# Performance work log

Measured on AMD Instinct MI355X. Metric: run time of the kernel, lower is better.

Reference implementation:

```python
import jax, jax.numpy as jnp
from jax import lax
import numpy as np

IMG_H = 14; IMG_W = 14
L = 21   # num_labels
M = 5    # num_mixture_filters
KL = 50  # local conv kernel
PL = 25  # local conv padding
HO = IMG_H + 2 * PL - KL + 1  # 15, locally-connected output size
CH = [(64, 3), (64, 64), (128, 64), (128, 128), (256, 128), (256, 256), (256, 256),
      (512, 256), (512, 512), (512, 512), (512, 512), (512, 512), (512, 512)]
DIL = [1, 1, 1, 1, 1, 1, 1, 1, 1, 1, 2, 2, 2]


def setup_inputs() -> dict:
    keys = iter(jax.random.split(jax.random.key(0), 80))
    def rnd(shape, s=0.05):
        return jax.random.normal(next(keys), shape, dtype=jnp.float32) * s
    d = {"x": jax.random.normal(next(keys), (2, 3, IMG_H, IMG_W), dtype=jnp.float32)}
    for i, (o, c) in enumerate(CH):
        d["w%d" % (i + 1)] = rnd((o, c, 3, 3))
        d["b%d" % (i + 1)] = rnd((o,))
    d["wf1"] = rnd((4096, 512, 7, 7), s=0.01); d["bf1"] = rnd((4096,))
    d["wf2"] = rnd((4096, 4096, 1, 1), s=0.01); d["bf2"] = rnd((4096,))
    d["wf3"] = rnd((L, 4096, 1, 1), s=0.01); d["bf3"] = rnd((L,))
    d["wl"] = rnd((HO, HO, L, L, KL, KL), s=0.01)  # per-position local-conv weights
    d["bl"] = rnd((L, HO, HO))
    d["wa"] = rnd((L, L)); d["ba"] = rnd((L,))
    d["wm"] = rnd((L * M, L, 9, 9, L)); d["bm"] = rnd((L * M,))
    d["wb"] = rnd((L * M, L * M)); d["bb"] = rnd((L * M,))
    return d


def _conv2d(x, w, b, pad, dil=1):
    y = lax.conv_general_dilated(x, w, (1, 1), [(pad, pad), (pad, pad)],
                                 rhs_dilation=(dil, dil),
                                 dimension_numbers=("NCHW", "OIHW", "NCHW"))
    return y + b[None, :, None, None]


def _maxpool2(x):
    return lax.reduce_window(x, -jnp.inf, lax.max, (1, 1, 2, 2), (1, 1, 2, 2), "VALID")


def _upsample_bilinear_ac(x, H, W):
    # UpsamplingBilinear2d == bilinear with align_corners=True
    def lerp(t, n_in, n_out, axis):
        src = jnp.arange(n_out, dtype=jnp.float32) * (float(n_in - 1) / max(n_out - 1, 1))
        i0 = jnp.clip(jnp.floor(src).astype(jnp.int32), 0, max(n_in - 2, 0))
        i1 = jnp.minimum(i0 + 1, n_in - 1)
        f = src - i0.astype(jnp.float32)
        shp = [1] * t.ndim; shp[axis] = n_out
        f = f.reshape(shp).astype(t.dtype)
        return jnp.take(t, i0, axis=axis) * (1 - f) + jnp.take(t, i1, axis=axis) * f
    return lerp(lerp(x, x.shape[2], H, 2), x.shape[3], W, 3)


def reference(x, w1, b1, w2, b2, w3, b3, w4, b4, w5, b5, w6, b6, w7, b7, w8, b8,
              w9, b9, w10, b10, w11, b11, w12, b12, w13, b13,
              wf1, bf1, wf2, bf2, wf3, bf3, wl, bl, wa, ba, wm, bm, wb, bb):
    ws = [w1, w2, w3, w4, w5, w6, w7, w8, w9, w10, w11, w12, w13]
    bs = [b1, b2, b3, b4, b5, b6, b7, b8, b9, b10, b11, b12, b13]
    h = x
    for i in range(13):
        h = jax.nn.relu(_conv2d(h, ws[i], bs[i], pad=DIL[i], dil=DIL[i]))
        if i in (1, 3, 6):  # MaxPool2d after VGG blocks 1,2,3
            h = _maxpool2(h)
    h = jax.nn.relu(_conv2d(h, wf1, bf1, pad=12, dil=4))  # 7x7 dilated FC-conv
    h = jax.nn.relu(_conv2d(h, wf2, bf2, pad=0))
    h = _conv2d(h, wf3, bf3, pad=0)                       # -> [B, L, h', w']
    h = jax.nn.sigmoid(_upsample_bilinear_ac(h, IMG_H, IMG_W))
    # Conv2dLocal: locally-connected 50x50 conv, per-position weights
    xp = jnp.pad(h, ((0, 0), (0, 0), (PL, PL), (PL, PL)))
    idx = jnp.arange(HO)[:, None] + jnp.arange(KL)[None, :]  # [HO, KL]
    p = xp[:, :, idx, :][:, :, :, :, idx]  # [B, C, HO, KL, HO, KL]
    h = jnp.einsum("bcisjt,ijocst->boij", p, wl) + bl[None]  # [B, L, HO, HO]
    # Linear over the label (channel) axis
    h = jnp.einsum("bchw,oc->bohw", h, wa) + ba[None, :, None, None]
    # Conv3d mixture head: label axis unsqueezed to depth-1 last spatial dim,
    # kernel (9, 9, L) with padding (4, 4, L//2) -> depth out = 1
    y = lax.conv_general_dilated(h[..., None], wm, (1, 1, 1),
                                 [(4, 4), (4, 4), (L // 2, L // 2)],
                                 dimension_numbers=("NCDHW", "OIDHW", "NCDHW"))
    h = y[..., 0] + bm[None, :, None, None]  # [B, L*M, HO, HO]
    h = jnp.einsum("bchw,oc->bohw", h, wb) + bb[None, :, None, None]
    # BlockMinPooling(kernel=M) over last dim: split into (M, W//M), min over block axis
    B_, C_, H_, W_ = h.shape
    h = h.reshape(B_, C_, H_, M, W_ // M).min(axis=3)  # [B, L*M, HO, HO//M]
    # AvgPool2d(kernel=1, stride=1, divisor_override=1) is the identity
    return jax.nn.softmax(h, axis=1)
```

## Files before the change

kernel.cpp:

```cpp
#include <hip/hip_runtime.h>
#include <math.h>

#define HO 15
#define LBL 21
#define MIX 5
#define LM 105
#define NB 256
#define NT 256
#define GSZ (NB * NT)
#define NWV (GSZ / 64)

struct Params {
    const float* x;
    const float* w[14]; const float* b[14];
    const float *wf1, *bf1, *wf2, *bf2, *wf3, *bf3;
    const float *wl, *bl, *wa, *ba, *wm, *bm, *wb, *bb;
    float *A, *B, *v, *h1, *h3, *out;
    float *wf1d, *wtd[6], *wmd;
    int* bar;
};

__device__ __forceinline__ float max4(float a, float b, float c, float d) {
    return fmaxf(fmaxf(a, b), fmaxf(c, d));
}

__device__ __forceinline__ void gbar(int* bar, int id) {
    __syncthreads();
    if (threadIdx.x == 0) {
        __threadfence();
        int* c = bar + id * 16;
        __hip_atomic_fetch_add(c, 1, __ATOMIC_RELAXED, __HIP_MEMORY_SCOPE_AGENT);
        while (__hip_atomic_load(c, __ATOMIC_RELAXED, __HIP_MEMORY_SCOPE_AGENT) < NB)
            __builtin_amdgcn_s_sleep(16);
        (void)__hip_atomic_load(c, __ATOMIC_ACQUIRE, __HIP_MEMORY_SCOPE_AGENT);
    }
    __syncthreads();
}

__device__ void extract(const float* __restrict__ src, float* __restrict__ dst,
                        int n, int stride, int off, int gtid) {
#pragma unroll 4
    for (int e = gtid; e < n; e += GSZ) dst[e] = src[(size_t)e * stride + off];
}

template <int Cin, int Cout, int Hi, int H, int POOL>
__device__ void wconv(const float* __restrict__ in, const float* __restrict__ w,
                      const float* __restrict__ bias, float* __restrict__ out,
                      int gw, int lane) {
    constexpr int CPL = Cin / 64;
    for (int idx = gw; idx < 2 * Cout * H * H; idx += NWV) {
        int x = idx % H; int t = idx / H;
        int y = t % H; t /= H;
        int o = t % Cout; int b = t / Cout;
        const float* ip = in + (size_t)b * Cin * Hi * Hi;
        float acc = 0.f;
#pragma unroll
        for (int cc = 0; cc < CPL; ++cc) {
            int c = lane + 64 * cc;
            const float* ic = ip + (size_t)c * Hi * Hi;
            const float* wc = w + ((size_t)o * Cin + c) * 9;
#pragma unroll
            for (int ky = 0; ky < 3; ++ky) {
                int yy = y + ky - 1;
                if (yy < 0 || yy >= H) continue;
#pragma unroll
                for (int kx = 0; kx < 3; ++kx) {
                    int xx = x + kx - 1;
                    if (xx < 0 || xx >= H) continue;
                    float val;
                    if (POOL == 1) {
                        val = ic[yy * Hi + xx];
                    } else {
                        const float* q = ic + (2 * yy) * Hi + 2 * xx;
                        val = max4(q[0], q[1], q[Hi], q[Hi + 1]);
                    }
                    acc += val * wc[ky * 3 + kx];
                }
            }
        }
#pragma unroll
        for (int off = 32; off; off >>= 1) acc += __shfl_xor(acc, off);
        if (lane == 0) out[idx] = fmaxf(acc + bias[o], 0.f);
    }
}

template <int Cin, int ACT, int POOLIN>
__device__ void mvdense(const float* __restrict__ in, const float* __restrict__ wd,
                        const float* __restrict__ bias, float* __restrict__ out,
                        int Cout, float* sin, int tid, int gw, int lane) {
    if (POOLIN) {
        for (int c = tid; c < 2 * Cin; c += NT) {
            const float* q = in + (size_t)c * 9;
            sin[c] = max4(q[0], q[1], q[3], q[4]);
        }
    } else {
        for (int c = tid; c < 2 * Cin; c += NT) sin[c] = in[c];
    }
    __syncthreads();
    constexpr int K = Cin / 64;
    for (int o = gw; o < Cout; o += NWV) {
        const float* wp = wd + (size_t)o * Cin + lane;
        float wr[K];
#pragma unroll
        for (int k = 0; k < K; ++k) wr[k] = wp[64 * k];
        float a0 = 0.f, a1 = 0.f;
#pragma unroll
        for (int k = 0; k < K; ++k) {
            a0 += wr[k] * sin[lane + 64 * k];
            a1 += wr[k] * sin[Cin + lane + 64 * k];
        }
#pragma unroll
        for (int off = 32; off; off >>= 1) {
            a0 += __shfl_xor(a0, off);
            a1 += __shfl_xor(a1, off);
        }
        if (lane == 0) {
            float bv = bias[o];
            a0 += bv; a1 += bv;
            if (ACT == 1) { a0 = fmaxf(a0, 0.f); a1 = fmaxf(a1, 0.f); }
            if (ACT == 2) { a0 = 1.f / (1.f + expf(-a0)); a1 = 1.f / (1.f + expf(-a1)); }
            out[o] = a0;
            out[Cout + o] = a1;
        }
    }
}

__device__ void localstage(const float* __restrict__ wl, const float* __restrict__ bl,
                           const float* __restrict__ v, float* __restrict__ h1,
                           int gw, int lane) {
    int e1 = lane + 64, e2 = lane + 128, e3 = lane + 192;
    int off0 = (lane / 14) * 50 + lane % 14;
    int off1 = (e1 / 14) * 50 + e1 % 14;
    int off2 = (e2 / 14) * 50 + e2 % 14;
    int off3 = (lane < 4) ? ((e3 / 14) * 50 + e3 % 14) : off0;
    float m3 = (lane < 4) ? 1.f : 0.f;
    for (int wk = gw; wk < LBL * HO * HO; wk += NWV) {
        int j = wk % HO; int t1 = wk / HO;
        int i = t1 % HO; int o = t1 / HO;
        int s0 = 25 - i, t0 = 25 - j;
        size_t base_ij = ((size_t)(i * HO + j) * LBL + o) * LBL;
        const float* pij = wl + base_ij * 2500 + s0 * 50 + t0;
        float a0 = 0.f, a1 = 0.f;
#pragma unroll 7
        for (int c = 0; c < LBL; ++c) {
            const float* p = pij + (size_t)c * 2500;
            float part = p[off0] + p[off1] + p[off2] + m3 * p[off3];
            a0 += v[c] * part;
            a1 += v[LBL + c] * part;
        }
#pragma unroll
        for (int off = 32; off; off >>= 1) {
            a0 += __shfl_xor(a0, off);
            a1 += __shfl_xor(a1, off);
        }
        if (lane == 0) {
            float bv = bl[(o * HO + i) * HO + j];
            h1[(size_t)(0 * LBL + o) * 225 + i * HO + j] = a0 + bv;
            h1[(size_t)(1 * LBL + o) * 225 + i * HO + j] = a1 + bv;
        }
    }
}

__device__ void ninestage(const float* __restrict__ h1, const float* __restrict__ wa,
                          const float* __restrict__ ba, const float* __restrict__ wmd,
                          const float* __restrict__ bm, float* __restrict__ h3,
                          float* smem, int tid) {
    int blk = blockIdx.x;
    if (blk >= 2 * LM) return;
    float* s1 = smem;
    float* s2 = smem + 4725;
    float* sw = smem + 9450;
    float* swa = smem + 11151;
    int b = blk / LM, o = blk % LM;
    for (int k = tid; k < 4725; k += NT) s1[k] = h1[(size_t)b * 4725 + k];
    for (int k = tid; k < 441; k += NT) swa[k] = wa[k];
    for (int k = tid; k < 1701; k += NT) sw[k] = wmd[(size_t)o * 1701 + k];
    __syncthreads();
    for (int k = tid; k < 4725; k += NT) {
        int c = k / 225, pix = k % 225;
        float acc = ba[c];
#pragma unroll 7
        for (int c2 = 0; c2 < LBL; ++c2)
            acc += swa[c * LBL + c2] * s1[c2 * 225 + pix];
        s2[k] = acc;
    }
    __syncthreads();
    if (tid >= 225) return;
    int i = tid / HO, j = tid % HO;
    float acc = bm[o];
    for (int c = 0; c < LBL; ++c) {
        const float* wp = sw + c * 81;
        const float* hp = s2 + c * 225;
#pragma unroll
        for (int di = 0; di < 9; ++di) {
            int y = i + di - 4;
            if (y < 0 || y >= HO) continue;
#pragma unroll
            for (int dj = 0; dj < 9; ++dj) {
                int x = j + dj - 4;
                if (x < 0 || x >= HO) continue;
                acc += hp[y * HO + x] * wp[di * 9 + dj];
            }
        }
    }
    h3[((size_t)b * LM + o) * 225 + tid] = acc;
}

__device__ void finalstage(const float* __restrict__ h3, const float* __restrict__ wbw,
                           const float* __restrict__ bbv, float* __restrict__ out,
                           float* smem, int tid) {
    int blk = blockIdx.x;
    if (blk >= 2 * HO * 3) return;
    float* sv = smem;
    float* sred = smem + 112;
    int k = blk % 3; int t = blk / 3; int i = t % HO; int b = t / HO;
    int o = tid;
    if (o < LM) {
        float mn = 3.4e38f;
        for (int mm = 0; mm < MIX; ++mm) {
            int j = mm * 3 + k;
            float acc = bbv[o];
            const float* hp = h3 + (size_t)b * LM * 225 + i * HO + j;
            const float* wp = wbw + o * LM;
#pragma unroll 5
            for (int c = 0; c < LM; ++c) acc += wp[c] * hp[(size_t)c * 225];
            mn = fminf(mn, acc);
        }
        sv[o] = mn;
    }
    __syncthreads();
    if (tid < 64) {
        float m = -3.4e38f;
        for (int c = tid; c < LM; c += 64) m = fmaxf(m, sv[c]);
#pragma unroll
        for (int off = 32; off; off >>= 1) m = fmaxf(m, __shfl_xor(m, off));
        if (tid == 0) sred[0] = m;
    }
    __syncthreads();
    if (o < LM) sv[o] = expf(sv[o] - sred[0]);
    __syncthreads();
    if (tid < 64) {
        float s = 0.f;
        for (int c = tid; c < LM; c += 64) s += sv[c];
#pragma unroll
        for (int off = 32; off; off >>= 1) s += __shfl_xor(s, off);
        if (tid == 0) sred[1] = s;
    }
    __syncthreads();
    if (o < LM) out[(((size_t)b * LM + o) * HO + i) * 3 + k] = sv[o] / sred[1];
}

__global__ __launch_bounds__(NT, 1) void mega(Params p) {
    const int tid = threadIdx.x;
    const int gtid = blockIdx.x * NT + tid;
    const int gw = gtid >> 6;
    const int lane = tid & 63;
    __shared__ float smem[11592];

    extract(p.wf1,   p.wf1d,   4096 * 512, 49, 24, gtid);
    extract(p.w[8],  p.wtd[0],  512 * 256,  9,  4, gtid);
    extract(p.w[9],  p.wtd[1],  512 * 512,  9,  4, gtid);
    extract(p.w[10], p.wtd[2],  512 * 512,  9,  4, gtid);
    extract(p.w[11], p.wtd[3],  512 * 512,  9,  4, gtid);
    extract(p.w[12], p.wtd[4],  512 * 512,  9,  4, gtid);
    extract(p.w[13], p.wtd[5],  512 * 512,  9,  4, gtid);
    extract(p.wm,    p.wmd,     105 * 1701, 21, 10, gtid);
    for (int idx = gtid; idx < 2 * 64 * 196; idx += GSZ) {
        int x = idx % 14; int t = idx / 14;
        int y = t % 14; t /= 14;
        int o = t % 64; int b = t / 64;
        const float* ip = p.x + (size_t)b * 3 * 196;
        const float* wp = p.w[1] + (size_t)o * 27;
        float acc = p.b[1][o];
#pragma unroll
        for (int c = 0; c < 3; ++c) {
            const float* ic = ip + c * 196;
            const float* wc = wp + c * 9;
#pragma unroll
            for (int ky = 0; ky < 3; ++ky) {
                int yy = y + ky - 1;
                if (yy < 0 || yy >= 14) continue;
#pragma unroll
                for (int kx = 0; kx < 3; ++kx) {
                    int xx = x + kx - 1;
                    if (xx < 0 || xx >= 14) continue;
                    acc += ic[yy * 14 + xx] * wc[ky * 3 + kx];
                }
            }
        }
        p.A[idx] = fmaxf(acc, 0.f);
    }
    gbar(p.bar, 0);

    wconv<64,  64, 14, 14, 1>(p.A, p.w[2], p.b[2], p.B, gw, lane);  gbar(p.bar, 1);
    wconv<64, 128, 14,  7, 2>(p.B, p.w[3], p.b[3], p.A, gw, lane);  gbar(p.bar, 2);
    wconv<128,128,  7,  7, 1>(p.A, p.w[4], p.b[4], p.B, gw, lane);  gbar(p.bar, 3);
    wconv<128,256,  7,  3, 2>(p.B, p.w[5], p.b[5], p.A, gw, lane);  gbar(p.bar, 4);
    wconv<256,256,  3,  3, 1>(p.A, p.w[6], p.b[6], p.B, gw, lane);  gbar(p.bar, 5);
    wconv<256,256,  3,  3, 1>(p.B, p.w[7], p.b[7], p.A, gw, lane);  gbar(p.bar, 6);

    mvdense<256, 1, 1>(p.A, p.wtd[0], p.b[8],  p.B, 512, smem, tid, gw, lane);  gbar(p.bar, 7);
    mvdense<512, 1, 0>(p.B, p.wtd[1], p.b[9],  p.A, 512, smem, tid, gw, lane);  gbar(p.bar, 8);
    mvdense<512, 1, 0>(p.A, p.wtd[2], p.b[10], p.B, 512, smem, tid, gw, lane);  gbar(p.bar, 9);
    mvdense<512, 1, 0>(p.B, p.wtd[3], p.b[11], p.A, 512, smem, tid, gw, lane);  gbar(p.bar, 10);
    mvdense<512, 1, 0>(p.A, p.wtd[4], p.b[12], p.B, 512, smem, tid, gw, lane);  gbar(p.bar, 11);
    mvdense<512, 1, 0>(p.B, p.wtd[5], p.b[13], p.A, 512, smem, tid, gw, lane);  gbar(p.bar, 12);
    mvdense<512, 1, 0>(p.A, p.wf1d,   p.bf1,   p.B, 4096, smem, tid, gw, lane); gbar(p.bar, 13);
    mvdense<4096,1, 0>(p.B, p.wf2,    p.bf2,   p.A, 4096, smem, tid, gw, lane); gbar(p.bar, 14);
    mvdense<4096,2, 0>(p.A, p.wf3,    p.bf3,   p.v, 21,   smem, tid, gw, lane); gbar(p.bar, 15);

    localstage(p.wl, p.bl, p.v, p.h1, gw, lane);                     gbar(p.bar, 16);
    ninestage(p.h1, p.wa, p.ba, p.wmd, p.bm, p.h3, smem, tid);       gbar(p.bar, 17);
    finalstage(p.h3, p.wb, p.bb, p.out, smem, tid);
}

extern "C" void kernel_launch(void* const* d_in, const int* in_sizes, int n_in,
                              void* d_out, int out_size, void* d_ws, size_t ws_size,
                              hipStream_t stream) {
    Params p;
    p.x = (const float*)d_in[0];
    for (int i = 1; i <= 13; ++i) {
        p.w[i] = (const float*)d_in[2 * i - 1];
        p.b[i] = (const float*)d_in[2 * i];
    }
    p.wf1 = (const float*)d_in[27]; p.bf1 = (const float*)d_in[28];
    p.wf2 = (const float*)d_in[29]; p.bf2 = (const float*)d_in[30];
    p.wf3 = (const float*)d_in[31]; p.bf3 = (const float*)d_in[32];
    p.wl  = (const float*)d_in[33]; p.bl  = (const float*)d_in[34];
    p.wa  = (const float*)d_in[35]; p.ba  = (const float*)d_in[36];
    p.wm  = (const float*)d_in[37]; p.bm  = (const float*)d_in[38];
    p.wb  = (const float*)d_in[39]; p.bb  = (const float*)d_in[40];

    float* wsf = (float*)d_ws;
    p.bar = (int*)d_ws;
    p.A    = wsf + 1024;
    p.B    = wsf + 1024 + 32768;
    p.v    = wsf + 1024 + 65536;
    p.h1   = wsf + 1024 + 65600;
    p.h3   = wsf + 1024 + 75072;
    p.wf1d = wsf + 1024 + 122432;
    float* base = p.wf1d + 2097152;
    p.wtd[0] = base;
    p.wtd[1] = base + 131072;
    p.wtd[2] = base + 131072 + 262144;
    p.wtd[3] = base + 131072 + 2 * 262144;
    p.wtd[4] = base + 131072 + 3 * 262144;
    p.wtd[5] = base + 131072 + 4 * 262144;
    p.wmd    = base + 131072 + 5 * 262144;
    p.out = (float*)d_out;

    hipMemsetAsync(d_ws, 0, 4096, stream);
    hipLaunchKernelGGL(mega, dim3(NB), dim3(NT), 0, stream, p);
}
```

Before: 668.7 us.

## Read center-tap weights directly with strides and vectorize large dense layers

Drops the up-front extraction pass that copied the centre taps of the conv/fc1/mixture weights into workspace. The dense stages now read those taps straight from the original tensors with a strided index, so every layer still runs but the extra copy and its global write traffic are gone. fc2 and fc3 get a float4 row-wise matrix-vector path. Block size also goes from 256 to 512 threads, which doubles the waves available per pass but raises register pressure under launch_bounds and changes smem loop strides. The strided reads fetch whole cache lines for one useful float each.

```diff
diff --git a/kernel.cpp b/kernel.cpp
--- a/kernel.cpp
+++ b/kernel.cpp
@@ -6,7 +6,7 @@
 #define MIX 5
 #define LM 105
 #define NB 256
-#define NT 256
+#define NT 512
 #define GSZ (NB * NT)
 #define NWV (GSZ / 64)
 
@@ -16,7 +16,6 @@
     const float *wf1, *bf1, *wf2, *bf2, *wf3, *bf3;
     const float *wl, *bl, *wa, *ba, *wm, *bm, *wb, *bb;
     float *A, *B, *v, *h1, *h3, *out;
-    float *wf1d, *wtd[6], *wmd;
     int* bar;
 };
 
@@ -35,12 +34,6 @@
         (void)__hip_atomic_load(c, __ATOMIC_ACQUIRE, __HIP_MEMORY_SCOPE_AGENT);
     }
     __syncthreads();
-}
-
-__device__ void extract(const float* __restrict__ src, float* __restrict__ dst,
-                        int n, int stride, int off, int gtid) {
-#pragma unroll 4
-    for (int e = gtid; e < n; e += GSZ) dst[e] = src[(size_t)e * stride + off];
 }
 
 template <int Cin, int Cout, int Hi, int H, int POOL>
@@ -85,9 +78,9 @@
 }
 
 template <int Cin, int ACT, int POOLIN>
-__device__ void mvdense(const float* __restrict__ in, const float* __restrict__ wd,
-                        const float* __restrict__ bias, float* __restrict__ out,
-                        int Cout, float* sin, int tid, int gw, int lane) {
+__device__ void mvtap(const float* __restrict__ in, const float* __restrict__ w,
+                      const float* __restrict__ bias, float* __restrict__ out,
+                      int Cout, int S, int F, float* sin, int tid, int gw, int lane) {
     if (POOLIN) {
         for (int c = tid; c < 2 * Cin; c += NT) {
             const float* q = in + (size_t)c * 9;
@@ -99,15 +92,53 @@
     __syncthreads();
     constexpr int K = Cin / 64;
     for (int o = gw; o < Cout; o += NWV) {
-        const float* wp = wd + (size_t)o * Cin + lane;
+        const float* wp = w + ((size_t)o * Cin + lane) * S + F;
         float wr[K];
 #pragma unroll
-        for (int k = 0; k < K; ++k) wr[k] = wp[64 * k];
+        for (int k = 0; k < K; ++k) wr[k] = wp[(size_t)(64 * S) * k];
         float a0 = 0.f, a1 = 0.f;
 #pragma unroll
         for (int k = 0; k < K; ++k) {
             a0 += wr[k] * sin[lane + 64 * k];
             a1 += wr[k] * sin[Cin + lane + 64 * k];
+        }
+#pragma unroll
+        for (int off = 32; off; off >>= 1) {
+            a0 += __shfl_xor(a0, off);
+            a1 += __shfl_xor(a1, off);
+        }
+        if (lane == 0) {
+            float bv = bias[o];
+            a0 += bv; a1 += bv;
+            if (ACT == 1) { a0 = fmaxf(a0, 0.f); a1 = fmaxf(a1, 0.f); }
+            if (ACT == 2) { a0 = 1.f / (1.f + expf(-a0)); a1 = 1.f / (1.f + expf(-a1)); }
+            out[o] = a0;
+            out[Cout + o] = a1;
+        }
+    }
+}
+
+template <int Cin, int ACT>
+__device__ void mvrow4(const float* __restrict__ in, const float* __restrict__ w,
+                       const float* __restrict__ bias, float* __restrict__ out,
+                       int Cout, float* sin, int tid, int gw, int lane) {
+    for (int c = tid; c < 2 * Cin; c += NT) sin[c] = in[c];
+    __syncthreads();
+    constexpr int K4 = Cin / 256;
+    const float4* s0 = (const float4*)sin;
+    const float4* s1 = (const float4*)(sin + Cin);
+    for (int o = gw; o < Cout; o += NWV) {
+        const float4* wp = (const float4*)(w + (size_t)o * Cin) + lane;
+        float4 wr[K4];
+#pragma unroll
+        for (int k = 0; k < K4; ++k) wr[k] = wp[64 * k];
+        float a0 = 0.f, a1 = 0.f;
+#pragma unroll
+        for (int k = 0; k < K4; ++k) {
+            float4 xv = s0[lane + 64 * k];
+            float4 yv = s1[lane + 64 * k];
+            a0 += wr[k].x * xv.x + wr[k].y * xv.y + wr[k].z * xv.z + wr[k].w * xv.w;
+            a1 += wr[k].x * yv.x + wr[k].y * yv.y + wr[k].z * yv.z + wr[k].w * yv.w;
         }
 #pragma unroll
         for (int off = 32; off; off >>= 1) {
@@ -162,7 +193,7 @@
 }
 
 __device__ void ninestage(const float* __restrict__ h1, const float* __restrict__ wa,
-                          const float* __restrict__ ba, const float* __restrict__ wmd,
+                          const float* __restrict__ ba, const float* __restrict__ wm,
                           const float* __restrict__ bm, float* __restrict__ h3,
                           float* smem, int tid) {
     int blk = blockIdx.x;
@@ -174,7 +205,7 @@
     int b = blk / LM, o = blk % LM;
     for (int k = tid; k < 4725; k += NT) s1[k] = h1[(size_t)b * 4725 + k];
     for (int k = tid; k < 441; k += NT) swa[k] = wa[k];
-    for (int k = tid; k < 1701; k += NT) sw[k] = wmd[(size_t)o * 1701 + k];
+    for (int k = tid; k < 1701; k += NT) sw[k] = wm[((size_t)o * 1701 + k) * LBL + 10];
     __syncthreads();
     for (int k = tid; k < 4725; k += NT) {
         int c = k / 225, pix = k % 225;
@@ -257,14 +288,6 @@
     const int lane = tid & 63;
     __shared__ float smem[11592];
 
-    extract(p.wf1,   p.wf1d,   4096 * 512, 49, 24, gtid);
-    extract(p.w[8],  p.wtd[0],  512 * 256,  9,  4, gtid);
-    extract(p.w[9],  p.wtd[1],  512 * 512,  9,  4, gtid);
-    extract(p.w[10], p.wtd[2],  512 * 512,  9,  4, gtid);
-    extract(p.w[11], p.wtd[3],  512 * 512,  9,  4, gtid);
-    extract(p.w[12], p.wtd[4],  512 * 512,  9,  4, gtid);
-    extract(p.w[13], p.wtd[5],  512 * 512,  9,  4, gtid);
-    extract(p.wm,    p.wmd,     105 * 1701, 21, 10, gtid);
     for (int idx = gtid; idx < 2 * 64 * 196; idx += GSZ) {
         int x = idx % 14; int t = idx / 14;
         int y = t % 14; t /= 14;
@@ -299,18 +322,18 @@
     wconv<256,256,  3,  3, 1>(p.A, p.w[6], p.b[6], p.B, gw, lane);  gbar(p.bar, 5);
     wconv<256,256,  3,  3, 1>(p.B, p.w[7], p.b[7], p.A, gw, lane);  gbar(p.bar, 6);
 
-    mvdense<256, 1, 1>(p.A, p.wtd[0], p.b[8],  p.B, 512, smem, tid, gw, lane);  gbar(p.bar, 7);
-    mvdense<512, 1, 0>(p.B, p.wtd[1], p.b[9],  p.A, 512, smem, tid, gw, lane);  gbar(p.bar, 8);
-    mvdense<512, 1, 0>(p.A, p.wtd[2], p.b[10], p.B, 512, smem, tid, gw, lane);  gbar(p.bar, 9);
-    mvdense<512, 1, 0>(p.B, p.wtd[3], p.b[11], p.A, 512, smem, tid, gw, lane);  gbar(p.bar, 10);
-    mvdense<512, 1, 0>(p.A, p.wtd[4], p.b[12], p.B, 512, smem, tid, gw, lane);  gbar(p.bar, 11);
-    mvdense<512, 1, 0>(p.B, p.wtd[5], p.b[13], p.A, 512, smem, tid, gw, lane);  gbar(p.bar, 12);
-    mvdense<512, 1, 0>(p.A, p.wf1d,   p.bf1,   p.B, 4096, smem, tid, gw, lane); gbar(p.bar, 13);
-    mvdense<4096,1, 0>(p.B, p.wf2,    p.bf2,   p.A, 4096, smem, tid, gw, lane); gbar(p.bar, 14);
-    mvdense<4096,2, 0>(p.A, p.wf3,    p.bf3,   p.v, 21,   smem, tid, gw, lane); gbar(p.bar, 15);
+    mvtap<256, 1, 1>(p.A, p.w[8],  p.b[8],  p.B, 512, 9, 4, smem, tid, gw, lane);   gbar(p.bar, 7);
+    mvtap<512, 1, 0>(p.B, p.w[9],  p.b[9],  p.A, 512, 9, 4, smem, tid, gw, lane);   gbar(p.bar, 8);
+    mvtap<512, 1, 0>(p.A, p.w[10], p.b[10], p.B, 512, 9, 4, smem, tid, gw, lane);   gbar(p.bar, 9);
+    mvtap<512, 1, 0>(p.B, p.w[11], p.b[11], p.A, 512, 9, 4, smem, tid, gw, lane);   gbar(p.bar, 10);
+    mvtap<512, 1, 0>(p.A, p.w[12], p.b[12], p.B, 512, 9, 4, smem, tid, gw, lane);   gbar(p.bar, 11);
+    mvtap<512, 1, 0>(p.B, p.w[13], p.b[13], p.A, 512, 9, 4, smem, tid, gw, lane);   gbar(p.bar, 12);
+    mvtap<512, 1, 0>(p.A, p.wf1, p.bf1, p.B, 4096, 49, 24, smem, tid, gw, lane);    gbar(p.bar, 13);
+    mvrow4<4096, 1>(p.B, p.wf2, p.bf2, p.A, 4096, smem, tid, gw, lane);             gbar(p.bar, 14);
+    mvrow4<4096, 2>(p.A, p.wf3, p.bf3, p.v, 21, smem, tid, gw, lane);               gbar(p.bar, 15);
 
     localstage(p.wl, p.bl, p.v, p.h1, gw, lane);                     gbar(p.bar, 16);
-    ninestage(p.h1, p.wa, p.ba, p.wmd, p.bm, p.h3, smem, tid);       gbar(p.bar, 17);
+    ninestage(p.h1, p.wa, p.ba, p.wm, p.bm, p.h3, smem, tid);        gbar(p.bar, 17);
     finalstage(p.h3, p.wb, p.bb, p.out, smem, tid);
 }
 
@@ -333,20 +356,11 @@
 
     float* wsf = (float*)d_ws;
     p.bar = (int*)d_ws;
-    p.A    = wsf + 1024;
-    p.B    = wsf + 1024 + 32768;
-    p.v    = wsf + 1024 + 65536;
-    p.h1   = wsf + 1024 + 65600;
-    p.h3   = wsf + 1024 + 75072;
-    p.wf1d = wsf + 1024 + 122432;
-    float* base = p.wf1d + 2097152;
-    p.wtd[0] = base;
-    p.wtd[1] = base + 131072;
-    p.wtd[2] = base + 131072 + 262144;
-    p.wtd[3] = base + 131072 + 2 * 262144;
-    p.wtd[4] = base + 131072 + 3 * 262144;
-    p.wtd[5] = base + 131072 + 4 * 262144;
-    p.wmd    = base + 131072 + 5 * 262144;
+    p.A  = wsf + 1024;
+    p.B  = wsf + 1024 + 32768;
+    p.v  = wsf + 1024 + 65536;
+    p.h1 = wsf + 1024 + 65600;
+    p.h3 = wsf + 1024 + 75072;
     p.out = (float*)d_out;
 
     hipMemsetAsync(d_ws, 0, 4096, stream);
```

New measurement: 630.2 us. -5.8%, faster.
